# Kernel optimization log

Hardware: AMD Instinct MI355X
Metric: run time of the kernel (lower is better)

Reference implementation:

```python
import jax, jax.numpy as jnp
import numpy as np

N, C, B = 32, 1024, 1024
EPS = 1e-12


def setup_inputs() -> dict:
    key = jax.random.key(0)
    k1, k2, k3 = jax.random.split(key, 3)
    X = jax.random.normal(k1, (N, C, B), dtype=jnp.float32)
    # xavier_uniform for square [C, C]: bound = sqrt(6/(C+C))
    bound = float(np.sqrt(6.0 / (C + C)))
    Wk = jax.random.uniform(k2, (C, C), minval=-bound, maxval=bound, dtype=jnp.float32)
    Wq = jax.random.uniform(k3, (C, C), minval=-bound, maxval=bound, dtype=jnp.float32)
    Wk0 = jnp.zeros((C, 1), dtype=jnp.float32)
    Wq0 = jnp.zeros((C, 1), dtype=jnp.float32)
    return {"X": X, "Wk": Wk, "Wq": Wq, "Wk0": Wk0, "Wq0": Wq0}


def reference(X, Wk, Wq, Wk0, Wq0):
    # X: [N, C, B]; Wk/Wq: [C, C]; Wk0/Wq0: [C, 1]
    K = jnp.einsum('cd,ndb->ncb', Wk, X) + Wk0  # [N, C, B]
    Q = jnp.einsum('cd,ndb->ncb', Wq, X) + Wq0  # [N, C, B]
    DK2 = jnp.sum(K * K, axis=1)                # [N, B]
    DQ2 = jnp.sum(Q * Q, axis=1)                # [N, B]
    DQK = jnp.sqrt(jnp.maximum(DQ2[:, :, None] * DK2[:, None, :], EPS))  # [N, B, B]
    Y = jnp.einsum('ncq,nck->nqk', Q, K) / DQK  # [N, B, B]
    SM = jax.nn.softmax(Y, axis=1)              # column-wise softmax (dim=1)
    Z = jnp.einsum('ncb,nbq->ncq', X, SM)       # [N, C, B]
    return Z
```

## Files before the change

kernel.cpp:

```cpp
#include <hip/hip_runtime.h>


typedef __bf16 bf16x8 __attribute__((ext_vector_type(8)));
typedef float  f32x4  __attribute__((ext_vector_type(4)));

#define LOAD16_LDS(g, l)                                                       \
  __builtin_amdgcn_global_load_lds(                                            \
      (const __attribute__((address_space(1))) void*)(g),                      \
      (__attribute__((address_space(3))) void*)(l), 16, 0, 0)

__global__ __launch_bounds__(256) void convert_w(
    const float* __restrict__ Wk, const float* __restrict__ Wq,
    const float* __restrict__ Wk0, const float* __restrict__ Wq0,
    __bf16* __restrict__ Wb, float* __restrict__ bias2) {
  int i = blockIdx.x * 256 + threadIdx.x;
  if (i < 1048576) Wb[i] = (__bf16)Wk[i];
  else             Wb[i] = (__bf16)Wq[i - 1048576];
  if (i < 1024) bias2[i] = Wk0[i];
  if (i >= 1048576 && i < 1048576 + 1024) bias2[1024 + (i - 1048576)] = Wq0[i - 1048576];
}

__global__ __launch_bounds__(256) void convert_x(
    const float* __restrict__ X, __bf16* __restrict__ Xb, __bf16* __restrict__ Xtb) {
  const int n = blockIdx.z;
  const int c0 = blockIdx.y * 32, b0 = blockIdx.x * 32;
  __shared__ float t[32][33];
  const int tx = threadIdx.x, ty = threadIdx.y;
  const float* Xn = X + (size_t)n * 1024 * 1024;
  __bf16* Xbn = Xb + (size_t)n * 1024 * 1024;
  __bf16* Xtn = Xtb + (size_t)n * 1024 * 1024;
#pragma unroll
  for (int i = 0; i < 4; ++i) {
    int c = c0 + ty + i * 8;
    float v = Xn[(size_t)c * 1024 + b0 + tx];
    Xbn[(size_t)c * 1024 + b0 + tx] = (__bf16)v;
    t[ty + i * 8][tx] = v;
  }
  __syncthreads();
#pragma unroll
  for (int i = 0; i < 4; ++i) {
    int b = b0 + ty + i * 8;
    Xtn[(size_t)b * 1024 + c0 + tx] = (__bf16)t[tx][ty + i * 8];
  }
}

template <int EPI>
__global__ __launch_bounds__(256) void gemm_nt(
    const __bf16* __restrict__ A, const __bf16* __restrict__ Bm,
    void* __restrict__ Out, int lda, int ldb, int ldo, int K,
    long long sA, long long sB, long long sO,
    const float* __restrict__ rowS, const float* __restrict__ colS,
    const float* __restrict__ bias,
    float* __restrict__ sqK, float* __restrict__ sqQ) {
  const int n = blockIdx.z;
  A += (size_t)n * sA;
  Bm += (size_t)n * sB;
  const int tileM = blockIdx.y * 128, tileN = blockIdx.x * 128;

  __shared__ __bf16 Al[128 * 32];
  __shared__ __bf16 Bl[128 * 32];

  const int tid = threadIdx.x, w = tid >> 6, lane = tid & 63;
  const int srow = lane >> 2;
  const int scol = ((lane & 3) ^ ((srow >> 1) & 3)) * 8;
  const int wr = (w >> 1) * 64, wc = (w & 1) * 64;
  const int r16 = lane & 15, quad = lane >> 4;

  const __bf16* gA0 = A + (size_t)(tileM + w * 32 + srow) * lda + scol;
  const __bf16* gA1 = gA0 + (size_t)16 * lda;
  const __bf16* gB0 = Bm + (size_t)(tileN + w * 32 + srow) * ldb + scol;
  const __bf16* gB1 = gB0 + (size_t)16 * ldb;
  __bf16* lA0 = &Al[(w * 32) * 32];
  __bf16* lA1 = &Al[(w * 32 + 16) * 32];
  __bf16* lB0 = &Bl[(w * 32) * 32];
  __bf16* lB1 = &Bl[(w * 32 + 16) * 32];

  f32x4 acc[4][4];
#pragma unroll
  for (int i = 0; i < 4; ++i)
#pragma unroll
    for (int j = 0; j < 4; ++j) acc[i][j] = (f32x4){0.f, 0.f, 0.f, 0.f};

  for (int k0 = 0; k0 < K; k0 += 32) {
    LOAD16_LDS(gA0, lA0);
    LOAD16_LDS(gA1, lA1);
    LOAD16_LDS(gB0, lB0);
    LOAD16_LDS(gB1, lB1);
    gA0 += 32; gA1 += 32; gB0 += 32; gB1 += 32;
    __syncthreads();

    bf16x8 af[4], bf[4];
#pragma unroll
    for (int i = 0; i < 4; ++i) {
      const int r = wr + i * 16 + r16;
      af[i] = *(const bf16x8*)&Al[r * 32 + ((quad ^ ((r >> 1) & 3)) * 8)];
    }
#pragma unroll
    for (int j = 0; j < 4; ++j) {
      const int r = wc + j * 16 + r16;
      bf[j] = *(const bf16x8*)&Bl[r * 32 + ((quad ^ ((r >> 1) & 3)) * 8)];
    }
#pragma unroll
    for (int i = 0; i < 4; ++i)
#pragma unroll
      for (int j = 0; j < 4; ++j)
        acc[i][j] = __builtin_amdgcn_mfma_f32_16x16x32_bf16(af[i], bf[j], acc[i][j], 0, 0, 0);
    __syncthreads();
  }

  if (EPI == 0) {
    float* sq = (tileN < 1024) ? sqK : sqQ;
#pragma unroll
    for (int i = 0; i < 4; ++i) {
#pragma unroll
      for (int t = 0; t < 4; ++t) {
        const int grow = tileM + wr + i * 16 + quad * 4 + t;
        float ss = 0.f;
#pragma unroll
        for (int j = 0; j < 4; ++j) {
          const int gcol = tileN + wc + j * 16 + r16;
          const __bf16 bv = (__bf16)(acc[i][j][t] + bias[gcol]);
          ((__bf16*)Out)[(size_t)n * sO + (size_t)grow * ldo + gcol] = bv;
          const float f = (float)bv;
          ss += f * f;
        }
        ss += __shfl_xor(ss, 1);
        ss += __shfl_xor(ss, 2);
        ss += __shfl_xor(ss, 4);
        ss += __shfl_xor(ss, 8);
        if (r16 == 0) atomicAdd(&sq[n * 1024 + grow], ss);
      }
    }
  } else if (EPI == 1) {
    float cs[4];
#pragma unroll
    for (int j = 0; j < 4; ++j)
      cs[j] = colS[n * 1024 + tileN + wc + j * 16 + r16];
#pragma unroll
    for (int i = 0; i < 4; ++i) {
#pragma unroll
      for (int t = 0; t < 4; ++t) {
        const int grow = tileM + wr + i * 16 + quad * 4 + t;
        const float rs = rowS[n * 1024 + grow];
        float ss = 0.f;
#pragma unroll
        for (int j = 0; j < 4; ++j) {
          const int gcol = tileN + wc + j * 16 + r16;
          const float y = acc[i][j][t] * rsqrtf(fmaxf(rs * cs[j], 1e-12f));
          const __bf16 e = (__bf16)__expf(y - 1.0f);
          ((__bf16*)Out)[(size_t)n * sO + (size_t)grow * ldo + gcol] = e;
          ss += (float)e;
        }
        ss += __shfl_xor(ss, 1);
        ss += __shfl_xor(ss, 2);
        ss += __shfl_xor(ss, 4);
        ss += __shfl_xor(ss, 8);
        if (r16 == 0) atomicAdd(&sqK[n * 1024 + grow], ss);
      }
    }
  } else {
    float inv[4];
#pragma unroll
    for (int j = 0; j < 4; ++j)
      inv[j] = 1.0f / colS[n * 1024 + tileN + wc + j * 16 + r16];
#pragma unroll
    for (int i = 0; i < 4; ++i)
#pragma unroll
      for (int j = 0; j < 4; ++j)
#pragma unroll
        for (int t = 0; t < 4; ++t) {
          const int grow = tileM + wr + i * 16 + quad * 4 + t;
          const int gcol = tileN + wc + j * 16 + r16;
          ((float*)Out)[(size_t)n * sO + (size_t)grow * ldo + gcol] =
              acc[i][j][t] * inv[j];
        }
  }
}

extern "C" void kernel_launch(void* const* d_in, const int* in_sizes, int n_in,
                              void* d_out, int out_size, void* d_ws, size_t ws_size,
                              hipStream_t stream) {
  const float* X   = (const float*)d_in[0];
  const float* Wk  = (const float*)d_in[1];
  const float* Wq  = (const float*)d_in[2];
  const float* Wk0 = (const float*)d_in[3];
  const float* Wq0 = (const float*)d_in[4];

  char* ws = (char*)d_ws;
  const size_t MB = 1ull << 20;
  __bf16* Xb   = (__bf16*)(ws);
  __bf16* Xtb  = (__bf16*)(ws + 64 * MB);
  __bf16* ET   = (__bf16*)(ws + 64 * MB);
  __bf16* Wb   = (__bf16*)(ws + 128 * MB);
  __bf16* KQT  = (__bf16*)(ws + 132 * MB);
  float*  DK2  = (float*)(ws + 260 * MB);
  float*  DQ2  = (float*)(ws + 260 * MB + 128 * 1024);
  float*  S    = (float*)(ws + 260 * MB + 256 * 1024);
  float*  bias2= (float*)(ws + 260 * MB + 384 * 1024);

  const long long M1 = 1024LL * 1024LL;

  hipMemsetAsync(DK2, 0, 3 * 128 * 1024, stream);

  convert_w<<<8192, 256, 0, stream>>>(Wk, Wq, Wk0, Wq0, Wb, bias2);
  convert_x<<<dim3(32, 32, 32), dim3(32, 8), 0, stream>>>(X, Xb, Xtb);

  gemm_nt<0><<<dim3(16, 8, 32), 256, 0, stream>>>(
      Xtb, Wb, KQT, 1024, 1024, 2048, 1024, M1, 0LL, 2 * M1,
      nullptr, nullptr, bias2, DK2, DQ2);

  gemm_nt<1><<<dim3(8, 8, 32), 256, 0, stream>>>(
      KQT, KQT + 1024, ET, 2048, 2048, 1024, 1024, 2 * M1, 2 * M1, M1,
      DK2, DQ2, nullptr, S, nullptr);

  gemm_nt<2><<<dim3(8, 8, 32), 256, 0, stream>>>(
      Xb, ET, (float*)d_out, 1024, 1024, 1024, 1024, M1, M1, M1,
      nullptr, S, nullptr, nullptr, nullptr);
}
```

Before: 699.1 us.

## Replace 128x128 GEMM with 256x256 double-buffered pipelined MFMA kernel

Replaces the simple single-stage 128x128-tile GEMM with a 512-thread, 256x256-tile kernel using 128KB of dynamic LDS for double buffering with a 64-wide K step. Global-to-LDS loads for the next stage are interleaved with the MFMA phases, using explicit vmcnt/lgkmcnt waits, barriers and setprio to overlap memory traffic with compute. The aim is higher arithmetic intensity per tile and hiding load latency. In exchange it takes far more registers and LDS, so only one block fits per CU, and the hand-ordered waits are fragile if they are wrong.

```diff
diff --git a/kernel.cpp b/kernel.cpp
--- a/kernel.cpp
+++ b/kernel.cpp
@@ -8,6 +8,17 @@
   __builtin_amdgcn_global_load_lds(                                            \
       (const __attribute__((address_space(1))) void*)(g),                      \
       (__attribute__((address_space(3))) void*)(l), 16, 0, 0)
+
+#define FENCE() asm volatile("" ::: "memory")
+#define SBAR()                                                                 \
+  do { FENCE(); __builtin_amdgcn_s_barrier(); FENCE(); } while (0)
+#define LGKM0()                                                                \
+  do { asm volatile("s_waitcnt lgkmcnt(0)" ::: "memory");                      \
+       __builtin_amdgcn_sched_barrier(0); } while (0)
+#define VMW(n)                                                                 \
+  do { asm volatile("s_waitcnt vmcnt(" #n ")" ::: "memory");                   \
+       __builtin_amdgcn_sched_barrier(0); } while (0)
+#define MFMA16(a, b, c) __builtin_amdgcn_mfma_f32_16x16x32_bf16((a), (b), (c), 0, 0, 0)
 
 __global__ __launch_bounds__(256) void convert_w(
     const float* __restrict__ Wk, const float* __restrict__ Wq,
@@ -45,81 +56,159 @@
 }
 
 template <int EPI>
-__global__ __launch_bounds__(256) void gemm_nt(
+__global__ __launch_bounds__(512) void gemm256(
     const __bf16* __restrict__ A, const __bf16* __restrict__ Bm,
     void* __restrict__ Out, int lda, int ldb, int ldo, int K,
     long long sA, long long sB, long long sO,
     const float* __restrict__ rowS, const float* __restrict__ colS,
     const float* __restrict__ bias,
-    float* __restrict__ sqK, float* __restrict__ sqQ) {
+    float* __restrict__ sq0, float* __restrict__ sq1) {
+  extern __shared__ char smem[];
   const int n = blockIdx.z;
   A += (size_t)n * sA;
   Bm += (size_t)n * sB;
-  const int tileM = blockIdx.y * 128, tileN = blockIdx.x * 128;
-
-  __shared__ __bf16 Al[128 * 32];
-  __shared__ __bf16 Bl[128 * 32];
-
-  const int tid = threadIdx.x, w = tid >> 6, lane = tid & 63;
-  const int srow = lane >> 2;
-  const int scol = ((lane & 3) ^ ((srow >> 1) & 3)) * 8;
-  const int wr = (w >> 1) * 64, wc = (w & 1) * 64;
-  const int r16 = lane & 15, quad = lane >> 4;
-
-  const __bf16* gA0 = A + (size_t)(tileM + w * 32 + srow) * lda + scol;
-  const __bf16* gA1 = gA0 + (size_t)16 * lda;
-  const __bf16* gB0 = Bm + (size_t)(tileN + w * 32 + srow) * ldb + scol;
-  const __bf16* gB1 = gB0 + (size_t)16 * ldb;
-  __bf16* lA0 = &Al[(w * 32) * 32];
-  __bf16* lA1 = &Al[(w * 32 + 16) * 32];
-  __bf16* lB0 = &Bl[(w * 32) * 32];
-  __bf16* lB1 = &Bl[(w * 32 + 16) * 32];
-
-  f32x4 acc[4][4];
-#pragma unroll
-  for (int i = 0; i < 4; ++i)
+  const int tileM = blockIdx.y * 256, tileN = blockIdx.x * 256;
+
+  const int tid = threadIdx.x;
+  const int w = tid >> 6, lane = tid & 63;
+  const int wm = w >> 2, wn = w & 3;
+  const int r16 = lane & 15, q16 = lane >> 4;
+  const int wb = w * 1024;
+
+  const int srow = tid >> 3;
+  const int scol8 = ((tid & 7) ^ (srow & 7)) * 8;
+  const __bf16* gA[4];
+  const __bf16* gB[4];
+#pragma unroll
+  for (int c = 0; c < 4; ++c) {
+    gA[c] = A + (size_t)(tileM + c * 64 + srow) * lda + scol8;
+    gB[c] = Bm + (size_t)(tileN + c * 64 + srow) * ldb + scol8;
+  }
+
+  const int sw = (r16 & 7) << 4;
+  const int cc0 = (q16 * 16) ^ sw;
+  const int cc1 = cc0 ^ 64;
+  const int aRow = (wm * 128 + r16) * 128;
+  const int bRow = (wn * 64 + r16) * 128;
+
+  f32x4 acc[8][4];
+#pragma unroll
+  for (int i = 0; i < 8; ++i)
 #pragma unroll
     for (int j = 0; j < 4; ++j) acc[i][j] = (f32x4){0.f, 0.f, 0.f, 0.f};
 
-  for (int k0 = 0; k0 < K; k0 += 32) {
-    LOAD16_LDS(gA0, lA0);
-    LOAD16_LDS(gA1, lA1);
-    LOAD16_LDS(gB0, lB0);
-    LOAD16_LDS(gB1, lB1);
-    gA0 += 32; gA1 += 32; gB0 += 32; gB1 += 32;
-    __syncthreads();
-
-    bf16x8 af[4], bf[4];
-#pragma unroll
-    for (int i = 0; i < 4; ++i) {
-      const int r = wr + i * 16 + r16;
-      af[i] = *(const bf16x8*)&Al[r * 32 + ((quad ^ ((r >> 1) & 3)) * 8)];
+  const int NT = K >> 6;
+
+  {
+    char* A0 = smem;
+    char* B0 = smem + 32768;
+    char* A1 = smem + 65536;
+    char* B1 = smem + 65536 + 32768;
+    LOAD16_LDS(gB[0], B0 + 0 * 8192 + wb);
+    LOAD16_LDS(gB[1], B0 + 1 * 8192 + wb);
+    FENCE();
+    LOAD16_LDS(gB[2], B0 + 2 * 8192 + wb);
+    LOAD16_LDS(gB[3], B0 + 3 * 8192 + wb);
+    FENCE();
+    LOAD16_LDS(gA[0], A0 + 0 * 8192 + wb);
+    LOAD16_LDS(gA[2], A0 + 2 * 8192 + wb);
+    FENCE();
+    LOAD16_LDS(gA[1], A0 + 1 * 8192 + wb);
+    LOAD16_LDS(gA[3], A0 + 3 * 8192 + wb);
+    FENCE();
+    LOAD16_LDS(gB[0] + 64, B1 + 0 * 8192 + wb);
+    LOAD16_LDS(gB[1] + 64, B1 + 1 * 8192 + wb);
+    FENCE();
+    LOAD16_LDS(gB[2] + 64, B1 + 2 * 8192 + wb);
+    LOAD16_LDS(gB[3] + 64, B1 + 3 * 8192 + wb);
+    FENCE();
+    LOAD16_LDS(gA[0] + 64, A1 + 0 * 8192 + wb);
+    LOAD16_LDS(gA[2] + 64, A1 + 2 * 8192 + wb);
+    VMW(6);
+    SBAR();
+  }
+
+  int kU3 = 64, kU0 = 128, kU1 = 128, kU2 = 128;
+
+  for (int t = 0; t < NT; ++t) {
+    char* Ab = smem + (size_t)((t & 1) * 65536);
+    char* Bb = Ab + 32768;
+    char* An = smem + (size_t)(((t & 1) ^ 1) * 65536);
+
+    bf16x8 bfr[4][2];
+#pragma unroll
+    for (int ni = 0; ni < 4; ++ni) {
+      bfr[ni][0] = *(const bf16x8*)(Bb + bRow + ni * 2048 + cc0);
+      bfr[ni][1] = *(const bf16x8*)(Bb + bRow + ni * 2048 + cc1);
     }
-#pragma unroll
-    for (int j = 0; j < 4; ++j) {
-      const int r = wc + j * 16 + r16;
-      bf[j] = *(const bf16x8*)&Bl[r * 32 + ((quad ^ ((r >> 1) & 3)) * 8)];
+
+#pragma unroll
+    for (int p = 0; p < 4; ++p) {
+      bf16x8 af[2][2];
+#pragma unroll
+      for (int j = 0; j < 2; ++j) {
+        af[j][0] = *(const bf16x8*)(Ab + aRow + (2 * p + j) * 2048 + cc0);
+        af[j][1] = *(const bf16x8*)(Ab + aRow + (2 * p + j) * 2048 + cc1);
+      }
+      if (p == 0) {
+        if (kU3 < K) {
+          LOAD16_LDS(gA[1] + kU3, An + 1 * 8192 + wb);
+          LOAD16_LDS(gA[3] + kU3, An + 3 * 8192 + wb);
+          kU3 += 64;
+        }
+      } else if (p == 1) {
+        if (kU0 < K) {
+          LOAD16_LDS(gB[0] + kU0, Bb + 0 * 8192 + wb);
+          LOAD16_LDS(gB[1] + kU0, Bb + 1 * 8192 + wb);
+          kU0 += 64;
+        }
+      } else if (p == 2) {
+        if (kU1 < K) {
+          LOAD16_LDS(gB[2] + kU1, Bb + 2 * 8192 + wb);
+          LOAD16_LDS(gB[3] + kU1, Bb + 3 * 8192 + wb);
+          kU1 += 64;
+        }
+      } else {
+        if (kU2 < K) {
+          LOAD16_LDS(gA[0] + kU2, Ab + 0 * 8192 + wb);
+          LOAD16_LDS(gA[2] + kU2, Ab + 2 * 8192 + wb);
+          kU2 += 64;
+        }
+        if (t < NT - 2) { VMW(6); } else { VMW(0); }
+      }
+      SBAR();
+      LGKM0();
+      __builtin_amdgcn_s_setprio(1);
+#pragma unroll
+      for (int ni = 0; ni < 4; ++ni) {
+#pragma unroll
+        for (int j = 0; j < 2; ++j) {
+          acc[2 * p + j][ni] = MFMA16(af[j][0], bfr[ni][0], acc[2 * p + j][ni]);
+          acc[2 * p + j][ni] = MFMA16(af[j][1], bfr[ni][1], acc[2 * p + j][ni]);
+        }
+      }
+      __builtin_amdgcn_s_setprio(0);
+      SBAR();
     }
-#pragma unroll
-    for (int i = 0; i < 4; ++i)
-#pragma unroll
-      for (int j = 0; j < 4; ++j)
-        acc[i][j] = __builtin_amdgcn_mfma_f32_16x16x32_bf16(af[i], bf[j], acc[i][j], 0, 0, 0);
-    __syncthreads();
-  }
-
+  }
+
+  const int rowBase = tileM + wm * 128;
+  const int colBase = tileN + wn * 64;
   if (EPI == 0) {
-    float* sq = (tileN < 1024) ? sqK : sqQ;
-#pragma unroll
-    for (int i = 0; i < 4; ++i) {
-#pragma unroll
-      for (int t = 0; t < 4; ++t) {
-        const int grow = tileM + wr + i * 16 + quad * 4 + t;
+    float* sqp = (tileN < 1024) ? sq0 : sq1;
+    float bs[4];
+#pragma unroll
+    for (int ni = 0; ni < 4; ++ni) bs[ni] = bias[colBase + ni * 16 + r16];
+#pragma unroll
+    for (int mi = 0; mi < 8; ++mi) {
+#pragma unroll
+      for (int t_ = 0; t_ < 4; ++t_) {
+        const int grow = rowBase + mi * 16 + q16 * 4 + t_;
         float ss = 0.f;
 #pragma unroll
-        for (int j = 0; j < 4; ++j) {
-          const int gcol = tileN + wc + j * 16 + r16;
-          const __bf16 bv = (__bf16)(acc[i][j][t] + bias[gcol]);
+        for (int ni = 0; ni < 4; ++ni) {
+          const int gcol = colBase + ni * 16 + r16;
+          const __bf16 bv = (__bf16)(acc[mi][ni][t_] + bs[ni]);
           ((__bf16*)Out)[(size_t)n * sO + (size_t)grow * ldo + gcol] = bv;
           const float f = (float)bv;
           ss += f * f;
@@ -128,25 +217,25 @@
         ss += __shfl_xor(ss, 2);
         ss += __shfl_xor(ss, 4);
         ss += __shfl_xor(ss, 8);
-        if (r16 == 0) atomicAdd(&sq[n * 1024 + grow], ss);
+        if (r16 == 0) atomicAdd(&sqp[n * 1024 + grow], ss);
       }
     }
   } else if (EPI == 1) {
     float cs[4];
 #pragma unroll
-    for (int j = 0; j < 4; ++j)
-      cs[j] = colS[n * 1024 + tileN + wc + j * 16 + r16];
-#pragma unroll
-    for (int i = 0; i < 4; ++i) {
-#pragma unroll
-      for (int t = 0; t < 4; ++t) {
-        const int grow = tileM + wr + i * 16 + quad * 4 + t;
+    for (int ni = 0; ni < 4; ++ni)
+      cs[ni] = colS[n * 1024 + colBase + ni * 16 + r16];
+#pragma unroll
+    for (int mi = 0; mi < 8; ++mi) {
+#pragma unroll
+      for (int t_ = 0; t_ < 4; ++t_) {
+        const int grow = rowBase + mi * 16 + q16 * 4 + t_;
         const float rs = rowS[n * 1024 + grow];
         float ss = 0.f;
 #pragma unroll
-        for (int j = 0; j < 4; ++j) {
-          const int gcol = tileN + wc + j * 16 + r16;
-          const float y = acc[i][j][t] * rsqrtf(fmaxf(rs * cs[j], 1e-12f));
+        for (int ni = 0; ni < 4; ++ni) {
+          const int gcol = colBase + ni * 16 + r16;
+          const float y = acc[mi][ni][t_] * rsqrtf(fmaxf(rs * cs[ni], 1e-12f));
           const __bf16 e = (__bf16)__expf(y - 1.0f);
           ((__bf16*)Out)[(size_t)n * sO + (size_t)grow * ldo + gcol] = e;
           ss += (float)e;
@@ -155,24 +244,24 @@
         ss += __shfl_xor(ss, 2);
         ss += __shfl_xor(ss, 4);
         ss += __shfl_xor(ss, 8);
-        if (r16 == 0) atomicAdd(&sqK[n * 1024 + grow], ss);
+        if (r16 == 0) atomicAdd(&sq0[n * 1024 + grow], ss);
       }
     }
   } else {
     float inv[4];
 #pragma unroll
-    for (int j = 0; j < 4; ++j)
-      inv[j] = 1.0f / colS[n * 1024 + tileN + wc + j * 16 + r16];
-#pragma unroll
-    for (int i = 0; i < 4; ++i)
-#pragma unroll
-      for (int j = 0; j < 4; ++j)
-#pragma unroll
-        for (int t = 0; t < 4; ++t) {
-          const int grow = tileM + wr + i * 16 + quad * 4 + t;
-          const int gcol = tileN + wc + j * 16 + r16;
+    for (int ni = 0; ni < 4; ++ni)
+      inv[ni] = 1.0f / colS[n * 1024 + colBase + ni * 16 + r16];
+#pragma unroll
+    for (int mi = 0; mi < 8; ++mi)
+#pragma unroll
+      for (int ni = 0; ni < 4; ++ni)
+#pragma unroll
+        for (int t_ = 0; t_ < 4; ++t_) {
+          const int grow = rowBase + mi * 16 + q16 * 4 + t_;
+          const int gcol = colBase + ni * 16 + r16;
           ((float*)Out)[(size_t)n * sO + (size_t)grow * ldo + gcol] =
-              acc[i][j][t] * inv[j];
+              acc[mi][ni][t_] * inv[ni];
         }
   }
 }
@@ -200,20 +289,27 @@
 
   const long long M1 = 1024LL * 1024LL;
 
+  hipFuncSetAttribute(reinterpret_cast<const void*>(&gemm256<0>),
+                      hipFuncAttributeMaxDynamicSharedMemorySize, 131072);
+  hipFuncSetAttribute(reinterpret_cast<const void*>(&gemm256<1>),
+                      hipFuncAttributeMaxDynamicSharedMemorySize, 131072);
+  hipFuncSetAttribute(reinterpret_cast<const void*>(&gemm256<2>),
+                      hipFuncAttributeMaxDynamicSharedMemorySize, 131072);
+
   hipMemsetAsync(DK2, 0, 3 * 128 * 1024, stream);
 
   convert_w<<<8192, 256, 0, stream>>>(Wk, Wq, Wk0, Wq0, Wb, bias2);
   convert_x<<<dim3(32, 32, 32), dim3(32, 8), 0, stream>>>(X, Xb, Xtb);
 
-  gemm_nt<0><<<dim3(16, 8, 32), 256, 0, stream>>>(
+  gemm256<0><<<dim3(8, 4, 32), 512, 131072, stream>>>(
       Xtb, Wb, KQT, 1024, 1024, 2048, 1024, M1, 0LL, 2 * M1,
       nullptr, nullptr, bias2, DK2, DQ2);
 
-  gemm_nt<1><<<dim3(8, 8, 32), 256, 0, stream>>>(
+  gemm256<1><<<dim3(4, 4, 32), 512, 131072, stream>>>(
       KQT, KQT + 1024, ET, 2048, 2048, 1024, 1024, 2 * M1, 2 * M1, M1,
       DK2, DQ2, nullptr, S, nullptr);
 
-  gemm_nt<2><<<dim3(8, 8, 32), 256, 0, stream>>>(
+  gemm256<2><<<dim3(4, 4, 32), 512, 131072, stream>>>(
       Xb, ET, (float*)d_out, 1024, 1024, 1024, 1024, M1, M1, M1,
       nullptr, S, nullptr, nullptr, nullptr);
 }
```

New measurement: 580.9 us. -16.9%, faster.
